# Kernel optimization log

Hardware: AMD Instinct MI355X
Metric: run time of the kernel (lower is better)

The kernel has to match this reference:

```python
import math
import jax, jax.numpy as jnp
import numpy as np

HIDDEN = 1024
HEADS = 16
HEAD_DIM = HIDDEN // HEADS
PRIME = 7
MAX_ITERS = 10
ENT_THRESH = 0.2
PRIME_SCALE = 1.0 / math.sqrt(PRIME * HEAD_DIM)
EPS = 1e-6


def setup_inputs() -> dict:
    key = jax.random.key(0)
    ks = jax.random.split(key, 6)
    B, S = 2, 2048
    w = 0.02
    return {
        "hidden_states": jax.random.normal(ks[0], (B, S, HIDDEN), jnp.float32),
        "q_w": jax.random.normal(ks[1], (HIDDEN, HIDDEN), jnp.float32) * w,
        "q_b": jnp.zeros((HIDDEN,), jnp.float32),
        "k_w": jax.random.normal(ks[2], (HIDDEN, HIDDEN), jnp.float32) * w,
        "k_b": jnp.zeros((HIDDEN,), jnp.float32),
        "v_w": jax.random.normal(ks[3], (HIDDEN, HIDDEN), jnp.float32) * w,
        "v_b": jnp.zeros((HIDDEN,), jnp.float32),
        "o_w": jax.random.normal(ks[4], (HIDDEN, HIDDEN), jnp.float32) * w,
        "o_b": jnp.zeros((HIDDEN,), jnp.float32),
        "attention_mask": jnp.ones((B, S), jnp.int32),
    }


def _split_heads(x):
    B, S, _ = x.shape
    return x.reshape(B, S, HEADS, HEAD_DIM).transpose(0, 2, 1, 3)


def reference(hidden_states, q_w, q_b, k_w, k_b, v_w, v_b, o_w, o_b, attention_mask):
    B, S, _ = hidden_states.shape
    # projections (torch Linear: x @ W^T + b)
    q = _split_heads(hidden_states @ q_w.T + q_b) * PRIME_SCALE  # [B,H,S,hd]
    k = _split_heads(hidden_states @ k_w.T + k_b)
    v = _split_heads(hidden_states @ v_w.T + v_b)

    scores = jnp.einsum("bhqd,bhkd->bhqk", q, k)  # [B,H,S,S]
    mask = attention_mask[:, None, None, :]
    scores = jnp.where(mask == 0, -jnp.inf, scores)
    attn = jax.nn.softmax(scores, axis=-1)  # dropout p=0 (eval)

    base = jnp.einsum("bhqk,bhkd->bhqd", attn, v)  # attention_weights @ v

    # entropy of the (fixed) attention weights: [B,H]
    entropy = -jnp.sum(attn * jnp.log(attn + EPS), axis=-1).mean(axis=-1)
    avg_entropy = entropy.mean()

    # loop never changes attn, so entropy is constant: either break at i=1 or run all
    full = base
    for i in range(1, MAX_ITERS):
        blend = 1.0 / (1.0 + math.exp(-i / MAX_ITERS))          # sigmoid(i/max)
        res_scale = 0.5 + 0.5 * blend                            # resonance scale
        full = (1.0 - blend) * full + blend * (res_scale * base)

    out_heads = jnp.where(avg_entropy < ENT_THRESH, base, full)  # [B,H,S,hd]

    merged = out_heads.transpose(0, 2, 1, 3).reshape(B, S, HIDDEN)
    return merged @ o_w.T + o_b
```

## Files before the change

### kernel.cpp

```cpp
#include <hip/hip_runtime.h>
#include <hip/hip_bf16.h>
#include <stdint.h>


#define PRIME_SCALE 0.047245559126654356f
#define LOG2E       1.4426950408889634f
#define LN2         0.6931471805599453f
#define QSCALE      (PRIME_SCALE * LOG2E)
#define BLEND_C     0.85096556f

#if __has_builtin(__builtin_amdgcn_exp2f)
#define EXP2(x) __builtin_amdgcn_exp2f(x)
#else
#define EXP2(x) exp2f(x)
#endif

typedef __attribute__((ext_vector_type(8))) short short8;
typedef __attribute__((ext_vector_type(4))) float f32x4;

__device__ __forceinline__ unsigned short f2bf(float x) {
    union { float f; unsigned int u; } v; v.f = x;
    unsigned int r = (v.u + 0x7fffu + ((v.u >> 16) & 1u)) >> 16;
    return (unsigned short)r;
}
__device__ __forceinline__ unsigned short f2bf_fast(float x) {
    union { float f; unsigned int u; } v; v.f = x;
    return (unsigned short)((v.u + 0x8000u) >> 16);
}
__device__ __forceinline__ float bf2f(unsigned short x) {
    union { unsigned int u; float f; } v; v.u = ((unsigned int)x) << 16;
    return v.f;
}

__device__ __forceinline__ void glds16(const unsigned short* g, unsigned short* l) {
    __builtin_amdgcn_global_load_lds((const __attribute__((address_space(1))) unsigned int*)g,
                                     (__attribute__((address_space(3))) unsigned int*)l,
                                     16, 0, 0);
}

__global__ void zero_out_f32(float* p, int n) {
    int i = blockIdx.x * 256 + threadIdx.x;
    if (i < n) p[i] = 0.f;
}

__global__ __launch_bounds__(256) void cvt5(
    const float* __restrict__ s0, const float* __restrict__ s1, const float* __restrict__ s2,
    const float* __restrict__ s3, const float* __restrict__ s4,
    unsigned short* __restrict__ d0, unsigned short* __restrict__ d1, unsigned short* __restrict__ d2,
    unsigned short* __restrict__ d3, unsigned short* __restrict__ d4, float* entp)
{
    if (blockIdx.x == 0 && threadIdx.x == 0) entp[0] = 0.f;
    unsigned int i = blockIdx.x * 256 + threadIdx.x;
    const float* s; unsigned short* d; unsigned int off;
    if (i < (1u << 20)) { s = s0; d = d0; off = i; }
    else {
        unsigned int j = i - (1u << 20);
        unsigned int sel = j >> 18; off = j & 0x3FFFFu;
        s = sel == 0 ? s1 : sel == 1 ? s2 : sel == 2 ? s3 : s4;
        d = sel == 0 ? d1 : sel == 1 ? d2 : sel == 2 ? d3 : d4;
    }
    float4 v = ((const float4*)s)[off];
    ushort4 p; p.x = f2bf(v.x); p.y = f2bf(v.y); p.z = f2bf(v.z); p.w = f2bf(v.w);
    ((ushort4*)d)[off] = p;
}

__global__ __launch_bounds__(256) void gemm_qkv(
    const unsigned short* __restrict__ hsb,
    const unsigned short* __restrict__ qwb, const unsigned short* __restrict__ kwb,
    const unsigned short* __restrict__ vwb,
    const float* __restrict__ qb, const float* __restrict__ kb, const float* __restrict__ vb,
    unsigned short* __restrict__ Qo, unsigned short* __restrict__ Ko, unsigned short* __restrict__ Vto)
{
    const int bid = blockIdx.x;
    const int op = bid >> 8, local = bid & 255;
    const unsigned short *A, *B; const float* bias; unsigned short* C;
    int m0, n0, ldc, biasRow; float scale;
    if (op == 0)      { A = hsb; B = qwb; bias = qb; C = Qo;  m0 = (local >> 3) * 128; n0 = (local & 7) * 128;  ldc = 1024; biasRow = 0; scale = QSCALE; }
    else if (op == 1) { A = hsb; B = kwb; bias = kb; C = Ko;  m0 = (local >> 3) * 128; n0 = (local & 7) * 128;  ldc = 1024; biasRow = 0; scale = 1.f; }
    else              { A = vwb; B = hsb; bias = vb; C = Vto; m0 = (local >> 5) * 128; n0 = (local & 31) * 128; ldc = 4096; biasRow = 1; scale = 1.f; }

    __shared__ unsigned short As[128 * 32];
    __shared__ unsigned short Bs[128 * 32];
    const int t = threadIdx.x, lane = t & 63, w = t >> 6;
    const int quad = lane >> 4, l15 = lane & 15;
    const int wr = (w >> 1) * 64, wc = (w & 1) * 64;
    const int srow = lane >> 2, scol = (lane & 3) * 8;

    f32x4 acc[4][4];
#pragma unroll
    for (int i = 0; i < 4; ++i)
#pragma unroll
        for (int j = 0; j < 4; ++j) acc[i][j] = (f32x4){0.f, 0.f, 0.f, 0.f};

    for (int kk = 0; kk < 32; ++kk) {
        const int k0 = kk * 32;
#pragma unroll
        for (int j = 0; j < 2; ++j) {
            int row = (w * 2 + j) * 16 + srow;
            glds16(&A[(size_t)(m0 + row) * 1024 + k0 + scol], &As[(w * 2 + j) * 512]);
            glds16(&B[(size_t)(n0 + row) * 1024 + k0 + scol], &Bs[(w * 2 + j) * 512]);
        }
        __syncthreads();
        short8 af[4], bf[4];
#pragma unroll
        for (int mt = 0; mt < 4; ++mt) af[mt] = *(const short8*)&As[(wr + mt * 16 + l15) * 32 + quad * 8];
#pragma unroll
        for (int nt = 0; nt < 4; ++nt) bf[nt] = *(const short8*)&Bs[(wc + nt * 16 + l15) * 32 + quad * 8];
#pragma unroll
        for (int mt = 0; mt < 4; ++mt)
#pragma unroll
            for (int nt = 0; nt < 4; ++nt)
                acc[mt][nt] = __builtin_amdgcn_mfma_f32_16x16x32_bf16(af[mt], bf[nt], acc[mt][nt], 0, 0, 0);
        __syncthreads();
    }
#pragma unroll
    for (int mt = 0; mt < 4; ++mt) {
#pragma unroll
        for (int nt = 0; nt < 4; ++nt) {
            int n = n0 + wc + nt * 16 + l15;
#pragma unroll
            for (int r = 0; r < 4; ++r) {
                int m = m0 + wr + mt * 16 + quad * 4 + r;
                float bval = biasRow ? bias[m] : bias[n];
                C[(size_t)m * ldc + n] = f2bf((acc[mt][nt][r] + bval) * scale);
            }
        }
    }
}

__global__ __launch_bounds__(256, 3) void flash_split(
    const unsigned short* __restrict__ Q,
    const unsigned short* __restrict__ K,
    const unsigned short* __restrict__ Vt,
    const int* __restrict__ mask,
    unsigned short* __restrict__ O0, unsigned short* __restrict__ O1,
    float* __restrict__ lpart, float* __restrict__ Tpart)
{
    const int qt = blockIdx.x;
    const int bh = blockIdx.y;
    const int z  = blockIdx.z;
    const int b = bh >> 4, h = bh & 15;
    const int t = threadIdx.x, lane = t & 63, w = t >> 6;
    const int quad = lane >> 4, l15 = lane & 15;
    const int r8 = lane >> 3, ch8 = lane & 7;
    const int kt0 = z * 16, kt1 = kt0 + 16;
    unsigned short* __restrict__ Opart = z ? O1 : O0;

    __shared__ unsigned short Qs[128 * 72];
    __shared__ unsigned short Ks[2][64 * 64];
    __shared__ unsigned short Vs[2][64 * 64];
    __shared__ unsigned int maskBits[64];

    const int* maskb = mask + b * 2048;
    {
        const int4* mp = (const int4*)(maskb + t * 8);
        int4 a = mp[0], c = mp[1];
        unsigned bits = (unsigned)(a.x != 0)       | ((unsigned)(a.y != 0) << 1)
                      | ((unsigned)(a.z != 0) << 2) | ((unsigned)(a.w != 0) << 3)
                      | ((unsigned)(c.x != 0) << 4) | ((unsigned)(c.y != 0) << 5)
                      | ((unsigned)(c.z != 0) << 6) | ((unsigned)(c.w != 0) << 7);
        ((unsigned char*)maskBits)[t] = (unsigned char)bits;
    }
    {
        const int row0 = w * 16;
#pragma unroll
        for (int i = 0; i < 2; ++i) {
            int row = row0 + i * 8 + r8;
            int c = ch8 ^ (row & 7);
            glds16(&K[(size_t)(b * 2048 + kt0 * 64 + row) * 1024 + h * 64 + c * 8], &Ks[0][(row0 + i * 8) * 64]);
            glds16(&Vt[(size_t)(h * 64 + row) * 4096 + b * 2048 + kt0 * 64 + c * 8], &Vs[0][(row0 + i * 8) * 64]);
        }
    }
#pragma unroll
    for (int i = 0; i < 4; ++i) {
        int f = i * 256 + t; int row = f >> 3, c = f & 7;
        uint4 v = *(const uint4*)&Q[(size_t)(b * 2048 + qt * 128 + row) * 1024 + h * 64 + c * 8];
        *(uint4*)&Qs[row * 72 + c * 8] = v;
    }
    __syncthreads();

    short8 qa[2][2];
#pragma unroll
    for (int st = 0; st < 2; ++st) {
        int qrow = w * 32 + st * 16 + l15;
        qa[st][0] = *(const short8*)&Qs[qrow * 72 + quad * 8];
        qa[st][1] = *(const short8*)&Qs[qrow * 72 + 32 + quad * 8];
    }
    unsigned short* Ps = Qs;

    float l_r[2][4], T_r[2][4];
    f32x4 o_acc[2][4];
#pragma unroll
    for (int st = 0; st < 2; ++st)
#pragma unroll
        for (int r = 0; r < 4; ++r) { l_r[st][r] = 0.f; T_r[st][r] = 0.f; }
#pragma unroll
    for (int st = 0; st < 2; ++st)
#pragma unroll
        for (int nt = 0; nt < 4; ++nt) o_acc[st][nt] = (f32x4){0.f, 0.f, 0.f, 0.f};

    for (int kt = kt0; kt < kt1; ++kt) {
        const int cur = kt & 1;
        if (kt < kt1 - 1) {
            const int kn = (kt + 1) * 64;
            const int row0 = w * 16;
#pragma unroll
            for (int i = 0; i < 2; ++i) {
                int row = row0 + i * 8 + r8;
                int c = ch8 ^ (row & 7);
                glds16(&K[(size_t)(b * 2048 + kn + row) * 1024 + h * 64 + c * 8], &Ks[cur ^ 1][(row0 + i * 8) * 64]);
                glds16(&Vt[(size_t)(h * 64 + row) * 4096 + b * 2048 + kn + c * 8], &Vs[cur ^ 1][(row0 + i * 8) * 64]);
            }
        }

        f32x4 sacc[2][4];
#pragma unroll
        for (int st = 0; st < 2; ++st)
#pragma unroll
            for (int nt = 0; nt < 4; ++nt) sacc[st][nt] = (f32x4){0.f, 0.f, 0.f, 0.f};
#pragma unroll
        for (int nt = 0; nt < 4; ++nt) {
            int krow = nt * 16 + l15;
            short8 kf0 = *(const short8*)&Ks[cur][krow * 64 + ((quad ^ (krow & 7)) * 8)];
            short8 kf1 = *(const short8*)&Ks[cur][krow * 64 + (((quad + 4) ^ (krow & 7)) * 8)];
#pragma unroll
            for (int st = 0; st < 2; ++st) {
                sacc[st][nt] = __builtin_amdgcn_mfma_f32_16x16x32_bf16(qa[st][0], kf0, sacc[st][nt], 0, 0, 0);
                sacc[st][nt] = __builtin_amdgcn_mfma_f32_16x16x32_bf16(qa[st][1], kf1, sacc[st][nt], 0, 0, 0);
            }
        }
        unsigned mw0 = maskBits[kt * 2], mw1 = maskBits[kt * 2 + 1];
        int mk[4];
        mk[0] = (mw0 >> l15) & 1;
        mk[1] = (mw0 >> (16 + l15)) & 1;
        mk[2] = (mw1 >> l15) & 1;
        mk[3] = (mw1 >> (16 + l15)) & 1;

#pragma unroll
        for (int st = 0; st < 2; ++st) {
#pragma unroll
            for (int r = 0; r < 4; ++r) {
                float s0 = mk[0] ? sacc[st][0][r] : -1.0e30f;
                float s1 = mk[1] ? sacc[st][1][r] : -1.0e30f;
                float s2 = mk[2] ? sacc[st][2][r] : -1.0e30f;
                float s3 = mk[3] ? sacc[st][3][r] : -1.0e30f;
                float p0 = EXP2(s0), p1 = EXP2(s1), p2 = EXP2(s2), p3 = EXP2(s3);
                l_r[st][r] += (p0 + p1) + (p2 + p3);
                T_r[st][r] += (p0 * s0 + p1 * s1) + (p2 * s2 + p3 * s3);
                int pbase = (w * 32 + st * 16 + quad * 4 + r) * 72 + l15;
                Ps[pbase]      = f2bf_fast(p0);
                Ps[pbase + 16] = f2bf_fast(p1);
                Ps[pbase + 32] = f2bf_fast(p2);
                Ps[pbase + 48] = f2bf_fast(p3);
            }
        }

#pragma unroll
        for (int ks = 0; ks < 2; ++ks) {
            short8 pa[2];
#pragma unroll
            for (int st = 0; st < 2; ++st)
                pa[st] = *(const short8*)&Ps[(w * 32 + st * 16 + l15) * 72 + ks * 32 + quad * 8];
#pragma unroll
            for (int nt = 0; nt < 4; ++nt) {
                int vrow = nt * 16 + l15;
                short8 vf = *(const short8*)&Vs[cur][vrow * 64 + ((((ks * 4 + quad)) ^ (vrow & 7)) * 8)];
#pragma unroll
                for (int st = 0; st < 2; ++st)
                    o_acc[st][nt] = __builtin_amdgcn_mfma_f32_16x16x32_bf16(pa[st], vf, o_acc[st][nt], 0, 0, 0);
            }
        }
        __syncthreads();
    }

#pragma unroll
    for (int st = 0; st < 2; ++st) {
#pragma unroll
        for (int r = 0; r < 4; ++r) {
            float l = l_r[st][r], T = T_r[st][r];
            l += __shfl_xor(l, 1); T += __shfl_xor(T, 1);
            l += __shfl_xor(l, 2); T += __shfl_xor(T, 2);
            l += __shfl_xor(l, 4); T += __shfl_xor(T, 4);
            l += __shfl_xor(l, 8); T += __shfl_xor(T, 8);
            int qrow = qt * 128 + w * 32 + st * 16 + quad * 4 + r;
            if (l15 == 0) {
                int li = z * 65536 + bh * 2048 + qrow;
                lpart[li] = l; Tpart[li] = T;
            }
            int mrow = b * 2048 + qrow;
#pragma unroll
            for (int nt = 0; nt < 4; ++nt)
                Opart[(size_t)mrow * 1024 + h * 64 + nt * 16 + l15] = f2bf_fast(o_acc[st][nt][r]);
        }
    }
}

__global__ __launch_bounds__(256) void combine_split(
    unsigned short* __restrict__ O0, const unsigned short* __restrict__ O1,
    const float* __restrict__ lpart)
{
    unsigned idx = blockIdx.x * 256 + threadIdx.x;
    int mrow = idx >> 8;
    int c4 = (idx & 255) << 2;
    int h = c4 >> 6;
    int b = mrow >> 11, qrow = mrow & 2047;
    int li = (b * 16 + h) * 2048 + qrow;
    float l = lpart[li] + lpart[65536 + li];
    float inv = 1.0f / l;

    ushort4 a = ((const ushort4*)O0)[idx];
    ushort4 c = ((const ushort4*)O1)[idx];
    ushort4 o;
    o.x = f2bf_fast((bf2f(a.x) + bf2f(c.x)) * inv);
    o.y = f2bf_fast((bf2f(a.y) + bf2f(c.y)) * inv);
    o.z = f2bf_fast((bf2f(a.z) + bf2f(c.z)) * inv);
    o.w = f2bf_fast((bf2f(a.w) + bf2f(c.w)) * inv);
    ((ushort4*)O0)[idx] = o;
}

__global__ __launch_bounds__(256) void entropy_k(
    const float* __restrict__ lpart, const float* __restrict__ Tpart,
    float* __restrict__ entp)
{
    __shared__ float wsum[4];
    int idx = blockIdx.x * 256 + threadIdx.x;
    float acc = 0.f;
#pragma unroll
    for (int i = 0; i < 4; ++i) {
        int r = idx * 4 + i;
        float l = lpart[r] + lpart[65536 + r];
        float T = Tpart[r] + Tpart[65536 + r];
        acc += __log2f(l) - T / l;
    }
    acc += __shfl_xor(acc, 1);
    acc += __shfl_xor(acc, 2);
    acc += __shfl_xor(acc, 4);
    acc += __shfl_xor(acc, 8);
    acc += __shfl_xor(acc, 16);
    acc += __shfl_xor(acc, 32);
    int lane = threadIdx.x & 63, w = threadIdx.x >> 6;
    if (lane == 0) wsum[w] = acc;
    __syncthreads();
    if (threadIdx.x == 0)
        atomicAdd(entp, LN2 * (wsum[0] + wsum[1] + wsum[2] + wsum[3]));
}

__global__ __launch_bounds__(256) void gemm_out_bf(
    const unsigned short* __restrict__ A, const unsigned short* __restrict__ Bw,
    const float* __restrict__ bias, const float* __restrict__ entp,
    float* __restrict__ C)
{
    const float avg = entp[0] * (1.0f / 65536.0f);
    const float scale = (avg < 0.2f) ? 1.0f : BLEND_C;

    const int m0 = blockIdx.x * 128;
    const int n0 = blockIdx.y * 64;
    __shared__ unsigned short As[128 * 32];
    __shared__ unsigned short Bs[64 * 32];
    const int t = threadIdx.x, lane = t & 63, w = t >> 6;
    const int quad = lane >> 4, l15 = lane & 15;
    const int wr = (w >> 1) * 64, wc = (w & 1) * 32;
    const int srow = lane >> 2, scol = (lane & 3) * 8;

    f32x4 acc[4][2];
#pragma unroll
    for (int i = 0; i < 4; ++i)
#pragma unroll
        for (int j = 0; j < 2; ++j) acc[i][j] = (f32x4){0.f, 0.f, 0.f, 0.f};

    for (int kk = 0; kk < 32; ++kk) {
        const int k0 = kk * 32;
#pragma unroll
        for (int j = 0; j < 2; ++j) {
            int row = (w * 2 + j) * 16 + srow;
            glds16(&A[(size_t)(m0 + row) * 1024 + k0 + scol], &As[(w * 2 + j) * 512]);
        }
        {
            int row = w * 16 + srow;
            glds16(&Bw[(size_t)(n0 + row) * 1024 + k0 + scol], &Bs[w * 512]);
        }
        __syncthreads();
        short8 af[4], bf[2];
#pragma unroll
        for (int mt = 0; mt < 4; ++mt) af[mt] = *(const short8*)&As[(wr + mt * 16 + l15) * 32 + quad * 8];
#pragma unroll
        for (int nt = 0; nt < 2; ++nt) bf[nt] = *(const short8*)&Bs[(wc + nt * 16 + l15) * 32 + quad * 8];
#pragma unroll
        for (int mt = 0; mt < 4; ++mt)
#pragma unroll
            for (int nt = 0; nt < 2; ++nt)
                acc[mt][nt] = __builtin_amdgcn_mfma_f32_16x16x32_bf16(af[mt], bf[nt], acc[mt][nt], 0, 0, 0);
        __syncthreads();
    }
#pragma unroll
    for (int mt = 0; mt < 4; ++mt) {
#pragma unroll
        for (int nt = 0; nt < 2; ++nt) {
            int n = n0 + wc + nt * 16 + l15;
#pragma unroll
            for (int r = 0; r < 4; ++r) {
                int m = m0 + wr + mt * 16 + quad * 4 + r;
                C[(size_t)m * 1024 + n] = scale * acc[mt][nt][r] + bias[n];
            }
        }
    }
}

extern "C" void kernel_launch(void* const* d_in, const int* in_sizes, int n_in,
                              void* d_out, int out_size, void* d_ws, size_t ws_size,
                              hipStream_t stream)
{
    const float* hs = (const float*)d_in[0];
    const float* qw = (const float*)d_in[1];
    const float* qb = (const float*)d_in[2];
    const float* kw = (const float*)d_in[3];
    const float* kb = (const float*)d_in[4];
    const float* vw = (const float*)d_in[5];
    const float* vb = (const float*)d_in[6];
    const float* ow = (const float*)d_in[7];
    const float* ob = (const float*)d_in[8];
    const int*   mask = (const int*)d_in[9];
    float* out = (float*)d_out;

    const size_t MB = 1024 * 1024;
    char* ws = (char*)d_ws;
    dim3 blk(256);

    if (ws_size >= 50 * MB) {
        unsigned short* hsb = (unsigned short*)(ws);
        unsigned short* Q   = (unsigned short*)(ws + 8 * MB);
        unsigned short* Kp  = (unsigned short*)(ws + 16 * MB);
        unsigned short* Vt  = (unsigned short*)(ws + 24 * MB);
        unsigned short* qwb = (unsigned short*)(ws + 32 * MB);
        unsigned short* kwb = (unsigned short*)(ws + 34 * MB);
        unsigned short* vwb = (unsigned short*)(ws + 36 * MB);
        unsigned short* owb = (unsigned short*)(ws + 38 * MB);
        float* entp         = (float*)(ws + 40 * MB);
        unsigned short* Op1 = (unsigned short*)(ws + 41 * MB);
        float* lpart        = (float*)(ws + 49 * MB);
        float* Tpart        = (float*)(ws + 49 * MB + 524288);
        unsigned short* Op0 = hsb;

        cvt5<<<dim3(8192), blk, 0, stream>>>(hs, qw, kw, vw, ow, hsb, qwb, kwb, vwb, owb, entp);
        gemm_qkv<<<dim3(768), blk, 0, stream>>>(hsb, qwb, kwb, vwb, qb, kb, vb, Q, Kp, Vt);
        flash_split<<<dim3(16, 32, 2), blk, 0, stream>>>(Q, Kp, Vt, mask, Op0, Op1, lpart, Tpart);
        combine_split<<<dim3(4096), blk, 0, stream>>>(Op0, Op1, lpart);
        entropy_k<<<dim3(64), blk, 0, stream>>>(lpart, Tpart, entp);
        gemm_out_bf<<<dim3(32, 16), blk, 0, stream>>>(Op0, owb, ob, entp, out);
    } else {
        zero_out_f32<<<dim3((out_size + 255) / 256), blk, 0, stream>>>(out, out_size);
    }
}
```

Baseline: 212.6 us.

## Transpose QK^T MFMA operands so each lane owns a query row; pack P stores

Swaps the A/B operands of the score MFMA so each lane holds four consecutive keys for a single query row. Per-row softmax sums then accumulate in one register per subtile and need only two cross-lane shuffles instead of four per row. P values are converted with the packed bf16 instruction and written to LDS as 8-byte vector stores instead of scalar 16-bit stores. It also raises wave priority around the MFMA blocks, and the mask bits are rearranged to match the new lane layout.

```diff
diff --git a/kernel.cpp b/kernel.cpp
--- a/kernel.cpp
+++ b/kernel.cpp
@@ -30,6 +30,11 @@
 __device__ __forceinline__ float bf2f(unsigned short x) {
     union { unsigned int u; float f; } v; v.u = ((unsigned int)x) << 16;
     return v.f;
+}
+__device__ __forceinline__ unsigned cvtpk_bf16(float lo, float hi) {
+    unsigned r;
+    asm("v_cvt_pk_bf16_f32 %0, %1, %2" : "=v"(r) : "v"(lo), "v"(hi));
+    return r;
 }
 
 __device__ __forceinline__ void glds16(const unsigned short* g, unsigned short* l) {
@@ -188,12 +193,8 @@
     }
     unsigned short* Ps = Qs;
 
-    float l_r[2][4], T_r[2][4];
+    float l_r[2] = {0.f, 0.f}, T_r[2] = {0.f, 0.f};
     f32x4 o_acc[2][4];
-#pragma unroll
-    for (int st = 0; st < 2; ++st)
-#pragma unroll
-        for (int r = 0; r < 4; ++r) { l_r[st][r] = 0.f; T_r[st][r] = 0.f; }
 #pragma unroll
     for (int st = 0; st < 2; ++st)
 #pragma unroll
@@ -213,11 +214,12 @@
             }
         }
 
-        f32x4 sacc[2][4];
-#pragma unroll
-        for (int st = 0; st < 2; ++st)
-#pragma unroll
-            for (int nt = 0; nt < 4; ++nt) sacc[st][nt] = (f32x4){0.f, 0.f, 0.f, 0.f};
+        f32x4 sacc[4][2];
+#pragma unroll
+        for (int nt = 0; nt < 4; ++nt)
+#pragma unroll
+            for (int st = 0; st < 2; ++st) sacc[nt][st] = (f32x4){0.f, 0.f, 0.f, 0.f};
+        __builtin_amdgcn_s_setprio(1);
 #pragma unroll
         for (int nt = 0; nt < 4; ++nt) {
             int krow = nt * 16 + l15;
@@ -225,33 +227,30 @@
             short8 kf1 = *(const short8*)&Ks[cur][krow * 64 + (((quad + 4) ^ (krow & 7)) * 8)];
 #pragma unroll
             for (int st = 0; st < 2; ++st) {
-                sacc[st][nt] = __builtin_amdgcn_mfma_f32_16x16x32_bf16(qa[st][0], kf0, sacc[st][nt], 0, 0, 0);
-                sacc[st][nt] = __builtin_amdgcn_mfma_f32_16x16x32_bf16(qa[st][1], kf1, sacc[st][nt], 0, 0, 0);
-            }
-        }
-        unsigned mw0 = maskBits[kt * 2], mw1 = maskBits[kt * 2 + 1];
-        int mk[4];
-        mk[0] = (mw0 >> l15) & 1;
-        mk[1] = (mw0 >> (16 + l15)) & 1;
-        mk[2] = (mw1 >> l15) & 1;
-        mk[3] = (mw1 >> (16 + l15)) & 1;
-
-#pragma unroll
-        for (int st = 0; st < 2; ++st) {
-#pragma unroll
-            for (int r = 0; r < 4; ++r) {
-                float s0 = mk[0] ? sacc[st][0][r] : -1.0e30f;
-                float s1 = mk[1] ? sacc[st][1][r] : -1.0e30f;
-                float s2 = mk[2] ? sacc[st][2][r] : -1.0e30f;
-                float s3 = mk[3] ? sacc[st][3][r] : -1.0e30f;
+                sacc[nt][st] = __builtin_amdgcn_mfma_f32_16x16x32_bf16(kf0, qa[st][0], sacc[nt][st], 0, 0, 0);
+                sacc[nt][st] = __builtin_amdgcn_mfma_f32_16x16x32_bf16(kf1, qa[st][1], sacc[nt][st], 0, 0, 0);
+            }
+        }
+        __builtin_amdgcn_s_setprio(0);
+
+        unsigned mwA = maskBits[kt * 2], mwB = maskBits[kt * 2 + 1];
+#pragma unroll
+        for (int nt = 0; nt < 4; ++nt) {
+            unsigned mw = (nt & 2) ? mwB : mwA;
+            unsigned mb = (mw >> (((nt & 1) << 4) + (quad << 2))) & 0xFu;
+#pragma unroll
+            for (int st = 0; st < 2; ++st) {
+                float s0 = (mb & 1u) ? sacc[nt][st][0] : -1.0e30f;
+                float s1 = (mb & 2u) ? sacc[nt][st][1] : -1.0e30f;
+                float s2 = (mb & 4u) ? sacc[nt][st][2] : -1.0e30f;
+                float s3 = (mb & 8u) ? sacc[nt][st][3] : -1.0e30f;
                 float p0 = EXP2(s0), p1 = EXP2(s1), p2 = EXP2(s2), p3 = EXP2(s3);
-                l_r[st][r] += (p0 + p1) + (p2 + p3);
-                T_r[st][r] += (p0 * s0 + p1 * s1) + (p2 * s2 + p3 * s3);
-                int pbase = (w * 32 + st * 16 + quad * 4 + r) * 72 + l15;
-                Ps[pbase]      = f2bf_fast(p0);
-                Ps[pbase + 16] = f2bf_fast(p1);
-                Ps[pbase + 32] = f2bf_fast(p2);
-                Ps[pbase + 48] = f2bf_fast(p3);
+                l_r[st] += (p0 + p1) + (p2 + p3);
+                T_r[st] += (p0 * s0 + p1 * s1) + (p2 * s2 + p3 * s3);
+                uint2 pk;
+                pk.x = cvtpk_bf16(p0, p1);
+                pk.y = cvtpk_bf16(p2, p3);
+                *(uint2*)&Ps[(w * 32 + st * 16 + l15) * 72 + nt * 16 + quad * 4] = pk;
             }
         }
 
@@ -261,6 +260,7 @@
 #pragma unroll
             for (int st = 0; st < 2; ++st)
                 pa[st] = *(const short8*)&Ps[(w * 32 + st * 16 + l15) * 72 + ks * 32 + quad * 8];
+            __builtin_amdgcn_s_setprio(1);
 #pragma unroll
             for (int nt = 0; nt < 4; ++nt) {
                 int vrow = nt * 16 + l15;
@@ -269,25 +269,24 @@
                 for (int st = 0; st < 2; ++st)
                     o_acc[st][nt] = __builtin_amdgcn_mfma_f32_16x16x32_bf16(pa[st], vf, o_acc[st][nt], 0, 0, 0);
             }
+            __builtin_amdgcn_s_setprio(0);
         }
         __syncthreads();
     }
 
 #pragma unroll
     for (int st = 0; st < 2; ++st) {
+        float l = l_r[st], T = T_r[st];
+        l += __shfl_xor(l, 16); T += __shfl_xor(T, 16);
+        l += __shfl_xor(l, 32); T += __shfl_xor(T, 32);
+        if (lane < 16) {
+            int qrow = qt * 128 + w * 32 + st * 16 + l15;
+            int li = z * 65536 + bh * 2048 + qrow;
+            lpart[li] = l; Tpart[li] = T;
+        }
 #pragma unroll
         for (int r = 0; r < 4; ++r) {
-            float l = l_r[st][r], T = T_r[st][r];
-            l += __shfl_xor(l, 1); T += __shfl_xor(T, 1);
-            l += __shfl_xor(l, 2); T += __shfl_xor(T, 2);
-            l += __shfl_xor(l, 4); T += __shfl_xor(T, 4);
-            l += __shfl_xor(l, 8); T += __shfl_xor(T, 8);
-            int qrow = qt * 128 + w * 32 + st * 16 + quad * 4 + r;
-            if (l15 == 0) {
-                int li = z * 65536 + bh * 2048 + qrow;
-                lpart[li] = l; Tpart[li] = T;
-            }
-            int mrow = b * 2048 + qrow;
+            int mrow = b * 2048 + qt * 128 + w * 32 + st * 16 + quad * 4 + r;
 #pragma unroll
             for (int nt = 0; nt < 4; ++nt)
                 Opart[(size_t)mrow * 1024 + h * 64 + nt * 16 + l15] = f2bf_fast(o_acc[st][nt][r]);
```

New measurement: 211.5 us. No clear change (-0.5%).
